# Kernel optimization log

Hardware: AMD Instinct MI355X
Metric: run time of the kernel (lower is better)

The kernel has to match this reference:

```python
import jax, jax.numpy as jnp
import numpy as np

N, D_IN, D_HID, K = 8192, 1024, 16384, 32


def setup_inputs() -> dict:
    key = jax.random.key(0)
    k1, k2, k3 = jax.random.split(key, 3)
    # Xavier-normal-ish scale for weights
    s_enc = (2.0 / (D_IN + D_HID)) ** 0.5
    x = jax.random.normal(k1, (N, D_IN), dtype=jnp.float32)
    W_enc = jax.random.normal(k2, (D_HID, D_IN), dtype=jnp.float32) * s_enc  # torch Linear(input->hidden) weight
    W_dec = jax.random.normal(k3, (D_IN, D_HID), dtype=jnp.float32) * s_enc  # torch Linear(hidden->input) weight
    return {"x": x, "W_enc": W_enc, "W_dec": W_dec}


def topk_activation(z, k):
    # keep top-k values along last dim, zero elsewhere (matches torch.topk + scatter_)
    vals, idx = jax.lax.top_k(z, k)  # [N, k]
    rows = jnp.arange(z.shape[0])[:, None]
    return jnp.zeros_like(z).at[rows, idx].set(vals)


def reference(x, W_enc, W_dec):
    z = jnp.maximum(x @ W_enc.T, 0.0)                 # encoder + ReLU, [N, D_HID]
    z_sparse = topk_activation(z, K)                  # [N, D_HID], k nonzeros/row
    x_hat = z_sparse @ W_dec.T                        # decoder, [N, D_IN]
    active = jnp.mean(jnp.sum((z_sparse > 0).astype(jnp.float32), axis=-1))
    return x_hat, z_sparse, z, active
```

## Files before the change

kernel.cpp:

```cpp
#include <hip/hip_runtime.h>


#define N_ROWS   8192
#define D_IN     1024
#define D_HID    16384
#define TOPK     32

typedef _Float16 half8  __attribute__((ext_vector_type(8)));
typedef _Float16 half4v __attribute__((ext_vector_type(4)));
typedef float    floatx4 __attribute__((ext_vector_type(4)));

#define WS_W1    ((size_t)0)
#define WS_W2    ((size_t)33554432)
#define WS_WDT   ((size_t)0)
#define WS_X1    ((size_t)67108864)
#define WS_X2    ((size_t)83886080)
#define WS_TOPV  ((size_t)100663296)
#define WS_TOPI  ((size_t)101711872)
#define WS_CNT   ((size_t)102760448)

#define OFF_XHAT ((size_t)0)
#define OFF_ZS   ((size_t)8388608)
#define OFF_Z    ((size_t)142606336)
#define OFF_ACT  ((size_t)276824064)

__device__ __forceinline__ void gload16(void* lds, const void* gptr) {
  __builtin_amdgcn_global_load_lds(
      (const __attribute__((address_space(1))) unsigned int*)gptr,
      (__attribute__((address_space(3))) unsigned int*)lds,
      16, 0, 0);
}

__global__ __launch_bounds__(256) void split_fp16(
    const float4* __restrict__ in, half4v* __restrict__ o1,
    half4v* __restrict__ o2, int n4)
{
  int i = blockIdx.x * 256 + threadIdx.x;
  int stride = gridDim.x * 256;
  for (; i < n4; i += stride) {
    float4 v = in[i];
    float a0 = v.x * 256.0f, a1 = v.y * 256.0f, a2 = v.z * 256.0f, a3 = v.w * 256.0f;
    half4v h1, h2;
    h1[0] = (_Float16)a0; h1[1] = (_Float16)a1; h1[2] = (_Float16)a2; h1[3] = (_Float16)a3;
    h2[0] = (_Float16)(a0 - (float)h1[0]);
    h2[1] = (_Float16)(a1 - (float)h1[1]);
    h2[2] = (_Float16)(a2 - (float)h1[2]);
    h2[3] = (_Float16)(a3 - (float)h1[3]);
    o1[i] = h1; o2[i] = h2;
  }
}

__global__ __launch_bounds__(256, 2) void gemm_enc(
    const _Float16* __restrict__ x1, const _Float16* __restrict__ x2,
    const _Float16* __restrict__ w1, const _Float16* __restrict__ w2,
    float* __restrict__ zout)
{
  __shared__ alignas(16) _Float16 sA1[128 * 32];
  __shared__ alignas(16) _Float16 sA2[128 * 32];
  __shared__ alignas(16) _Float16 sB1[128 * 32];
  __shared__ alignas(16) _Float16 sB2[128 * 32];

  int bid    = blockIdx.x;
  int cid    = bid >> 6;
  int within = bid & 63;
  int cm     = cid & 7;
  int cn     = cid >> 3;
  int mblk   = cm * 8 + (within & 7);
  int nblk   = cn * 8 + (within >> 3);

  int tid  = threadIdx.x;
  int wid  = tid >> 6, lane = tid & 63;
  int wm   = wid >> 1, wn = wid & 1;

  int c0    = wid * 2;
  int srow0 = lane >> 2;
  int skh   = (lane & 3) * 8;

  const size_t arow0 = (size_t)mblk * 128;
  const size_t brow0 = (size_t)nblk * 128;

  floatx4 acc[4][4];
#pragma unroll
  for (int t = 0; t < 4; t++)
#pragma unroll
    for (int u = 0; u < 4; u++) acc[t][u] = (floatx4)0.0f;

  int arow = wm * 64 + (lane & 15);
  int brow = wn * 64 + (lane & 15);
  int koff = (lane >> 4) * 8;

  for (int kb = 0; kb < D_IN / 32; ++kb) {
    __syncthreads();
#pragma unroll
    for (int rep = 0; rep < 2; ++rep) {
      int c = c0 + rep;
      int r = c * 16 + srow0;
      size_t ga = (arow0 + r) * D_IN + kb * 32 + skh;
      size_t gb = (brow0 + r) * D_IN + kb * 32 + skh;
      gload16((char*)sA1 + c * 1024, x1 + ga);
      gload16((char*)sA2 + c * 1024, x2 + ga);
      gload16((char*)sB1 + c * 1024, w1 + gb);
      gload16((char*)sB2 + c * 1024, w2 + gb);
    }
    __syncthreads();

    half8 a1f[4], a2f[4], b1f[4], b2f[4];
#pragma unroll
    for (int t = 0; t < 4; t++) {
      a1f[t] = *(const half8*)&sA1[(arow + t * 16) * 32 + koff];
      a2f[t] = *(const half8*)&sA2[(arow + t * 16) * 32 + koff];
      b1f[t] = *(const half8*)&sB1[(brow + t * 16) * 32 + koff];
      b2f[t] = *(const half8*)&sB2[(brow + t * 16) * 32 + koff];
    }
#pragma unroll
    for (int t = 0; t < 4; t++)
#pragma unroll
      for (int u = 0; u < 4; u++) {
        acc[t][u] = __builtin_amdgcn_mfma_f32_16x16x32_f16(a1f[t], b1f[u], acc[t][u], 0, 0, 0);
        acc[t][u] = __builtin_amdgcn_mfma_f32_16x16x32_f16(a1f[t], b2f[u], acc[t][u], 0, 0, 0);
        acc[t][u] = __builtin_amdgcn_mfma_f32_16x16x32_f16(a2f[t], b1f[u], acc[t][u], 0, 0, 0);
      }
  }

  int crow = (lane >> 4) * 4;
  int ccol = lane & 15;
  const float s = 1.0f / 65536.0f;
#pragma unroll
  for (int t = 0; t < 4; t++) {
    size_t grow = (size_t)mblk * 128 + wm * 64 + t * 16 + crow;
#pragma unroll
    for (int u = 0; u < 4; u++) {
      size_t gcol = (size_t)nblk * 128 + wn * 64 + u * 16 + ccol;
#pragma unroll
      for (int r = 0; r < 4; r++) {
        float v = acc[t][u][r] * s;
        v = v > 0.0f ? v : 0.0f;
        zout[(grow + r) * D_HID + gcol] = v;
      }
    }
  }
}

__global__ __launch_bounds__(256) void zerofill(
    float4* __restrict__ p, unsigned n4, unsigned* __restrict__ cnt)
{
  unsigned i = blockIdx.x * 256 + threadIdx.x;
  if (i == 0) *cnt = 0u;
  float4 z = make_float4(0.f, 0.f, 0.f, 0.f);
  for (; i < n4; i += gridDim.x * 256) p[i] = z;
}

#define BETTER(v1, i1, v2, i2) ((v1) > (v2) || ((v1) == (v2) && (i1) < (i2)))
#define NBINS 2048
#define CAND_CAP 1024

__global__ __launch_bounds__(256) void topk_rows(
    const float* __restrict__ z, float* __restrict__ z_sparse,
    float* __restrict__ topv, int* __restrict__ topi,
    unsigned* __restrict__ counter)
{
  int row = blockIdx.x;
  int tid = threadIdx.x;
  const float* zr = z + (size_t)row * D_HID;

  __shared__ unsigned hist[NBINS];
  __shared__ unsigned csum[256];
  __shared__ float    cv[CAND_CAP];
  __shared__ int      ci[CAND_CAP];
  __shared__ int      sB;
  __shared__ unsigned ccnt;
  __shared__ unsigned blk_pos;

#pragma unroll
  for (int i = tid; i < NBINS; i += 256) hist[i] = 0u;
  if (tid == 0) { ccnt = 0u; blk_pos = 0u; }
  __syncthreads();

  float4 vreg[16];
  unsigned lo = 0u;
#pragma unroll
  for (int s = 0; s < 16; ++s) {
    vreg[s] = *(const float4*)&zr[s * 1024 + tid * 4];
  }
#pragma unroll
  for (int s = 0; s < 16; ++s) {
    float vs[4] = {vreg[s].x, vreg[s].y, vreg[s].z, vreg[s].w};
#pragma unroll
    for (int c = 0; c < 4; ++c) {
      unsigned b = __float_as_uint(vs[c]) >> 21;
      if (b == 0u) ++lo;
      else atomicAdd(&hist[b], 1u);
    }
  }
  if (lo) atomicAdd(&hist[0], lo);
  __syncthreads();

  unsigned csl = 0u;
#pragma unroll
  for (int j = 0; j < 8; ++j) csl += hist[tid * 8 + j];
  csum[tid] = csl;
  __syncthreads();
#pragma unroll
  for (int off = 1; off < 256; off <<= 1) {
    unsigned v = (tid + off < 256) ? csum[tid + off] : 0u;
    __syncthreads();
    csum[tid] += v;
    __syncthreads();
  }
  {
    unsigned above = (tid < 255) ? csum[tid + 1] : 0u;
    unsigned run = above;
#pragma unroll
    for (int j = 7; j >= 0; --j) {
      int bin = tid * 8 + j;
      unsigned h = hist[bin];
      if (run < (unsigned)TOPK && run + h >= (unsigned)TOPK) sB = bin;
      run += h;
    }
  }
  __syncthreads();
  unsigned B = (unsigned)(sB > 0 ? sB : 1);
#pragma unroll
  for (int s = 0; s < 16; ++s) {
    float vs[4] = {vreg[s].x, vreg[s].y, vreg[s].z, vreg[s].w};
#pragma unroll
    for (int c = 0; c < 4; ++c) {
      unsigned u = __float_as_uint(vs[c]);
      if ((u >> 21) >= B) {
        unsigned pos = atomicAdd(&ccnt, 1u);
        if (pos < CAND_CAP) { cv[pos] = vs[c]; ci[pos] = s * 1024 + tid * 4 + c; }
      }
    }
  }
  __syncthreads();

  int C = (int)(ccnt < (unsigned)CAND_CAP ? ccnt : (unsigned)CAND_CAP);
  for (int p = tid; p < C; p += 256) {
    float v = cv[p]; int ix = ci[p];
    int rank = 0;
    for (int q = 0; q < C; ++q) {
      if (BETTER(cv[q], ci[q], v, ix)) ++rank;
    }
    if (rank < TOPK) {
      topv[row * TOPK + rank] = v;
      topi[row * TOPK + rank] = ix;
      z_sparse[(size_t)row * D_HID + ix] = v;
      if (v > 0.0f) atomicAdd(&blk_pos, 1u);
    }
  }
  __syncthreads();
  if (tid == 0) atomicAdd(counter, blk_pos);
}

__global__ __launch_bounds__(256) void transpose_wdec(
    const float* __restrict__ wd, float* __restrict__ wdt)
{
  __shared__ float t[32][33];
  int bx = blockIdx.x;
  int by = blockIdx.y;
  int tx = threadIdx.x & 31, ty = threadIdx.x >> 5;
#pragma unroll
  for (int r = 0; r < 4; r++) {
    int c = by * 32 + ty + r * 8;
    int j = bx * 32 + tx;
    t[ty + r * 8][tx] = wd[(size_t)c * D_HID + j];
  }
  __syncthreads();
#pragma unroll
  for (int r = 0; r < 4; r++) {
    int j = bx * 32 + ty + r * 8;
    int c = by * 32 + tx;
    wdt[(size_t)j * D_IN + c] = t[tx][ty + r * 8];
  }
}

__global__ __launch_bounds__(256) void decode(
    const float* __restrict__ topv, const int* __restrict__ topi,
    const float* __restrict__ wdt, float* __restrict__ xhat)
{
  int row = blockIdx.x;
  int tid = threadIdx.x;
  __shared__ float vv[TOPK]; __shared__ int ii[TOPK];
  if (tid < TOPK) { vv[tid] = topv[row * TOPK + tid]; ii[tid] = topi[row * TOPK + tid]; }
  __syncthreads();
  float ax = 0.f, ay = 0.f, az = 0.f, aw = 0.f;
  int c = tid * 4;
#pragma unroll 4
  for (int j = 0; j < TOPK; j++) {
    float v = vv[j];
    float4 w = *(const float4*)&wdt[(size_t)ii[j] * D_IN + c];
    ax += v * w.x; ay += v * w.y; az += v * w.z; aw += v * w.w;
  }
  float4 o = make_float4(ax, ay, az, aw);
  *(float4*)&xhat[(size_t)row * D_IN + c] = o;
}

__global__ void finalize_active(const unsigned* __restrict__ cnt, float* __restrict__ out)
{
  if (threadIdx.x == 0) out[0] = (float)(*cnt) * (1.0f / (float)N_ROWS);
}

extern "C" void kernel_launch(void* const* d_in, const int* in_sizes, int n_in,
                              void* d_out, int out_size, void* d_ws, size_t ws_size,
                              hipStream_t stream)
{
  const float* x     = (const float*)d_in[0];
  const float* W_enc = (const float*)d_in[1];
  const float* W_dec = (const float*)d_in[2];
  float* out = (float*)d_out;
  char*  ws  = (char*)d_ws;

  _Float16* x1 = (_Float16*)(ws + WS_X1);
  _Float16* x2 = (_Float16*)(ws + WS_X2);
  _Float16* w1 = (_Float16*)(ws + WS_W1);
  _Float16* w2 = (_Float16*)(ws + WS_W2);
  float*    wdt  = (float*)(ws + WS_WDT);
  float*    topv = (float*)(ws + WS_TOPV);
  int*      topi = (int*)(ws + WS_TOPI);
  unsigned* cnt  = (unsigned*)(ws + WS_CNT);

  float* xhat = out + OFF_XHAT;
  float* zsp  = out + OFF_ZS;
  float* z    = out + OFF_Z;
  float* act  = out + OFF_ACT;

  split_fp16<<<1024, 256, 0, stream>>>((const float4*)x, (half4v*)x1, (half4v*)x2,
                                       N_ROWS * D_IN / 4);
  split_fp16<<<2048, 256, 0, stream>>>((const float4*)W_enc, (half4v*)w1, (half4v*)w2,
                                       D_HID * D_IN / 4);
  gemm_enc<<<8192, 256, 0, stream>>>(x1, x2, w1, w2, z);
  zerofill<<<4096, 256, 0, stream>>>((float4*)zsp, (unsigned)(N_ROWS * (D_HID / 4)), cnt);
  topk_rows<<<N_ROWS, 256, 0, stream>>>(z, zsp, topv, topi, cnt);
  transpose_wdec<<<dim3(512, 32), 256, 0, stream>>>(W_dec, wdt);
  decode<<<N_ROWS, 256, 0, stream>>>(topv, topi, wdt, xhat);
  finalize_active<<<1, 64, 0, stream>>>(cnt, act);
}
```

Baseline: 2.169 ms.

## Double-buffer encoder GEMM LDS loads and fuse z_sparse zero-fill into top-k

The encoder GEMM now double-buffers its LDS tiles: the next K-slice is prefetched with global_load_lds while MFMAs run on the current one, leaving one barrier per iteration instead of two. The separate zerofill kernel is removed. Each top-k block zeroes its own z_sparse row before writing the selected values, and a tiny init kernel resets the counter. The top-k kernel also gets an occupancy hint in launch_bounds. LDS use in the GEMM doubles to 64KB per block, which may reduce occupancy. The zeroing stores inside the top-k kernel rely on the same threads writing the winning values later, after a barrier.

```diff
diff --git a/kernel.cpp b/kernel.cpp
--- a/kernel.cpp
+++ b/kernel.cpp
@@ -29,6 +29,11 @@
       (const __attribute__((address_space(1))) unsigned int*)gptr,
       (__attribute__((address_space(3))) unsigned int*)lds,
       16, 0, 0);
+}
+
+__global__ __launch_bounds__(64) void init_cnt(unsigned* __restrict__ cnt)
+{
+  if (threadIdx.x == 0) *cnt = 0u;
 }
 
 __global__ __launch_bounds__(256) void split_fp16(
@@ -55,10 +60,10 @@
     const _Float16* __restrict__ w1, const _Float16* __restrict__ w2,
     float* __restrict__ zout)
 {
-  __shared__ alignas(16) _Float16 sA1[128 * 32];
-  __shared__ alignas(16) _Float16 sA2[128 * 32];
-  __shared__ alignas(16) _Float16 sB1[128 * 32];
-  __shared__ alignas(16) _Float16 sB2[128 * 32];
+  __shared__ alignas(16) _Float16 sA1[2][128 * 32];
+  __shared__ alignas(16) _Float16 sA2[2][128 * 32];
+  __shared__ alignas(16) _Float16 sB1[2][128 * 32];
+  __shared__ alignas(16) _Float16 sB2[2][128 * 32];
 
   int bid    = blockIdx.x;
   int cid    = bid >> 6;
@@ -89,28 +94,35 @@
   int brow = wn * 64 + (lane & 15);
   int koff = (lane >> 4) * 8;
 
+#define STAGE(buf, kb)                                                  \
+  do {                                                                  \
+    _Pragma("unroll")                                                   \
+    for (int rep = 0; rep < 2; ++rep) {                                 \
+      int c = c0 + rep;                                                 \
+      int r = c * 16 + srow0;                                           \
+      size_t ga = (arow0 + r) * D_IN + (size_t)(kb) * 32 + skh;         \
+      size_t gb = (brow0 + r) * D_IN + (size_t)(kb) * 32 + skh;         \
+      gload16((char*)&sA1[buf][0] + c * 1024, x1 + ga);                 \
+      gload16((char*)&sA2[buf][0] + c * 1024, x2 + ga);                 \
+      gload16((char*)&sB1[buf][0] + c * 1024, w1 + gb);                 \
+      gload16((char*)&sB2[buf][0] + c * 1024, w2 + gb);                 \
+    }                                                                   \
+  } while (0)
+
+  STAGE(0, 0);
+  __syncthreads();
+
+  int cur = 0;
   for (int kb = 0; kb < D_IN / 32; ++kb) {
-    __syncthreads();
-#pragma unroll
-    for (int rep = 0; rep < 2; ++rep) {
-      int c = c0 + rep;
-      int r = c * 16 + srow0;
-      size_t ga = (arow0 + r) * D_IN + kb * 32 + skh;
-      size_t gb = (brow0 + r) * D_IN + kb * 32 + skh;
-      gload16((char*)sA1 + c * 1024, x1 + ga);
-      gload16((char*)sA2 + c * 1024, x2 + ga);
-      gload16((char*)sB1 + c * 1024, w1 + gb);
-      gload16((char*)sB2 + c * 1024, w2 + gb);
-    }
-    __syncthreads();
+    if (kb + 1 < D_IN / 32) STAGE(cur ^ 1, kb + 1);
 
     half8 a1f[4], a2f[4], b1f[4], b2f[4];
 #pragma unroll
     for (int t = 0; t < 4; t++) {
-      a1f[t] = *(const half8*)&sA1[(arow + t * 16) * 32 + koff];
-      a2f[t] = *(const half8*)&sA2[(arow + t * 16) * 32 + koff];
-      b1f[t] = *(const half8*)&sB1[(brow + t * 16) * 32 + koff];
-      b2f[t] = *(const half8*)&sB2[(brow + t * 16) * 32 + koff];
+      a1f[t] = *(const half8*)&sA1[cur][(arow + t * 16) * 32 + koff];
+      a2f[t] = *(const half8*)&sA2[cur][(arow + t * 16) * 32 + koff];
+      b1f[t] = *(const half8*)&sB1[cur][(brow + t * 16) * 32 + koff];
+      b2f[t] = *(const half8*)&sB2[cur][(brow + t * 16) * 32 + koff];
     }
 #pragma unroll
     for (int t = 0; t < 4; t++)
@@ -120,7 +132,11 @@
         acc[t][u] = __builtin_amdgcn_mfma_f32_16x16x32_f16(a1f[t], b2f[u], acc[t][u], 0, 0, 0);
         acc[t][u] = __builtin_amdgcn_mfma_f32_16x16x32_f16(a2f[t], b1f[u], acc[t][u], 0, 0, 0);
       }
-  }
+
+    __syncthreads();
+    cur ^= 1;
+  }
+#undef STAGE
 
   int crow = (lane >> 4) * 4;
   int ccol = lane & 15;
@@ -141,20 +157,11 @@
   }
 }
 
-__global__ __launch_bounds__(256) void zerofill(
-    float4* __restrict__ p, unsigned n4, unsigned* __restrict__ cnt)
-{
-  unsigned i = blockIdx.x * 256 + threadIdx.x;
-  if (i == 0) *cnt = 0u;
-  float4 z = make_float4(0.f, 0.f, 0.f, 0.f);
-  for (; i < n4; i += gridDim.x * 256) p[i] = z;
-}
-
 #define BETTER(v1, i1, v2, i2) ((v1) > (v2) || ((v1) == (v2) && (i1) < (i2)))
 #define NBINS 2048
 #define CAND_CAP 1024
 
-__global__ __launch_bounds__(256) void topk_rows(
+__global__ __launch_bounds__(256, 4) void topk_rows(
     const float* __restrict__ z, float* __restrict__ z_sparse,
     float* __restrict__ topv, int* __restrict__ topi,
     unsigned* __restrict__ counter)
@@ -162,6 +169,7 @@
   int row = blockIdx.x;
   int tid = threadIdx.x;
   const float* zr = z + (size_t)row * D_HID;
+  float*       zo = z_sparse + (size_t)row * D_HID;
 
   __shared__ unsigned hist[NBINS];
   __shared__ unsigned csum[256];
@@ -173,7 +181,11 @@
 
 #pragma unroll
   for (int i = tid; i < NBINS; i += 256) hist[i] = 0u;
-  if (tid == 0) { ccnt = 0u; blk_pos = 0u; }
+  if (tid == 0) { ccnt = 0u; blk_pos = 0u; sB = 1; }
+
+  float4 zz = make_float4(0.f, 0.f, 0.f, 0.f);
+#pragma unroll
+  for (int s = 0; s < 16; ++s) *(float4*)&zo[s * 1024 + tid * 4] = zz;
   __syncthreads();
 
   float4 vreg[16];
@@ -220,6 +232,7 @@
   }
   __syncthreads();
   unsigned B = (unsigned)(sB > 0 ? sB : 1);
+
 #pragma unroll
   for (int s = 0; s < 16; ++s) {
     float vs[4] = {vreg[s].x, vreg[s].y, vreg[s].z, vreg[s].w};
@@ -244,7 +257,7 @@
     if (rank < TOPK) {
       topv[row * TOPK + rank] = v;
       topi[row * TOPK + rank] = ix;
-      z_sparse[(size_t)row * D_HID + ix] = v;
+      zo[ix] = v;
       if (v > 0.0f) atomicAdd(&blk_pos, 1u);
     }
   }
@@ -324,12 +337,12 @@
   float* z    = out + OFF_Z;
   float* act  = out + OFF_ACT;
 
+  init_cnt<<<1, 64, 0, stream>>>(cnt);
   split_fp16<<<1024, 256, 0, stream>>>((const float4*)x, (half4v*)x1, (half4v*)x2,
                                        N_ROWS * D_IN / 4);
   split_fp16<<<2048, 256, 0, stream>>>((const float4*)W_enc, (half4v*)w1, (half4v*)w2,
                                        D_HID * D_IN / 4);
   gemm_enc<<<8192, 256, 0, stream>>>(x1, x2, w1, w2, z);
-  zerofill<<<4096, 256, 0, stream>>>((float4*)zsp, (unsigned)(N_ROWS * (D_HID / 4)), cnt);
   topk_rows<<<N_ROWS, 256, 0, stream>>>(z, zsp, topv, topi, cnt);
   transpose_wdec<<<dim3(512, 32), 256, 0, stream>>>(W_dec, wdt);
   decode<<<N_ROWS, 256, 0, stream>>>(topv, topi, wdt, xhat);
```

New measurement: 2.409 ms. +11.1%, slower.
